# Kernel optimization log

Hardware: AMD Instinct MI355X
Metric: run time of the kernel (lower is better)

The kernel has to match this reference:

```python
import jax, jax.numpy as jnp
import numpy as np

# Module hyper-parameters (from create_with_implicit_mesh defaults)
KERNEL_RADIUS = 4
KERNEL_SIGMA2 = 0.5
EPS = 1e-8


def _forward_shift(src, flow):
    """Flow-based forward splatting with Gaussian-kernel scatter-add.

    Each source pixel at integer grid location (x, y) lands at the continuous
    target position p = (x + u, y + v). Its value is splatted onto all target
    pixels within KERNEL_RADIUS of p with weight exp(-||t - p||^2 / (2*sigma2)),
    accumulated atomically into weighted-image / weight / mask buffers.
    """
    B, C, H, W = src.shape
    HW = H * W
    R = KERNEL_RADIUS
    dt = src.dtype

    xs = jnp.arange(W, dtype=dt)
    ys = jnp.arange(H, dtype=dt)
    px = (xs[None, None, :] + flow[:, 0]).reshape(B, HW)   # continuous landing x
    py = (ys[None, :, None] + flow[:, 1]).reshape(B, HW)   # continuous landing y
    bx = jnp.floor(px).astype(jnp.int32)                   # base integer target
    by = jnp.floor(py).astype(jnp.int32)

    src_f = src.reshape(B, C, HW)
    acc_wI = jnp.zeros((B, C, HW), dt)
    acc_w = jnp.zeros((B, HW), dt)

    b2 = jnp.arange(B)[:, None]                 # (B,1) for (B,HW) scatter
    b3 = jnp.arange(B)[:, None, None]           # (B,1,1) for (B,C,HW) scatter
    c3 = jnp.arange(C)[None, :, None]           # (1,C,1)

    r2 = jnp.asarray(R * R, dt)
    for dy in range(-R, R + 1):
        for dx in range(-R, R + 1):
            tx = bx + dx
            ty = by + dy
            fx = tx.astype(dt)
            fy = ty.astype(dt)
            d2 = (fx - px) ** 2 + (fy - py) ** 2
            valid = (tx >= 0) & (tx < W) & (ty >= 0) & (ty < H) & (d2 <= r2)
            w = jnp.exp(-d2 / (2.0 * KERNEL_SIGMA2)) * valid.astype(dt)  # (B,HW)
            idx = jnp.clip(ty, 0, H - 1) * W + jnp.clip(tx, 0, W - 1)    # (B,HW)
            acc_w = acc_w.at[b2, idx].add(w)
            acc_wI = acc_wI.at[b3, c3, idx[:, None, :]].add(w[:, None, :] * src_f)

    w_img = acc_w.reshape(B, 1, H, W)
    out_img = acc_wI.reshape(B, C, H, W) / (w_img + EPS)
    mask = (w_img > 0).astype(dt)
    return out_img, mask


def setup_inputs() -> dict:
    key = jax.random.key(0)
    k1, k2 = jax.random.split(key)
    B, C, H, W = 4, 3, 720, 1280
    src_image = jax.random.normal(k1, (B, C, H, W), dtype=jnp.float32)
    flow_src_to_tar = jax.random.normal(k2, (B, 2, H, W), dtype=jnp.float32)
    return {"src_image": src_image, "flow_src_to_tar": flow_src_to_tar}


def reference(src_image, flow_src_to_tar):
    return _forward_shift(src_image, flow_src_to_tar)
```

## Files before the change

kernel.cpp:

```cpp
#include <hip/hip_runtime.h>
#include <hip/hip_fp16.h>

constexpr int B_N = 4;
constexpr int C_N = 3;
constexpr int H_IMG = 720;
constexpr int W_IMG = 1280;
constexpr int HW = H_IMG * W_IMG;

constexpr int TW = 64, TH = 64;
constexpr int HALO = 7;
constexpr int CW = TW + 2 * HALO;
constexpr int CH = TH + 2 * HALO;
constexpr int PITCH = 79;
constexpr int PLANE = CH * PITCH;
constexpr float FLOW_MAX = 3.5f;
constexpr float LOG2E = 1.44269504f;
constexpr float MARKER = 30.0f;

#define K1 0.36787944117144233f
#define K3 0.049787068367863944f
#define K5 0.006737946999085467f
#define K7 0.0009118819655545162f

__global__ __launch_bounds__(256, 2)
void gather_kernel(const float* __restrict__ src, const float* __restrict__ flow,
                   float* __restrict__ out) {
    __shared__ __half2 UV[PLANE];
    __shared__ __half2 S01[PLANE];
    __shared__ __half  S2[PLANE];

    const int b = blockIdx.z;
    const int tx0 = blockIdx.x * TW;
    const int ty0 = blockIdx.y * TH;
    const int cx0 = tx0 - HALO, cy0 = ty0 - HALO;

    const float* __restrict__ up = flow + (size_t)(b * 2) * HW;
    const float* __restrict__ vp = up + HW;
    const float* __restrict__ sp = src + (size_t)(b * 3) * HW;

    for (int idx = threadIdx.x; idx < CH * CW; idx += 256) {
        const int cr = idx / CW, cx = idx - cr * CW;
        const int gx = cx0 + cx, gy = cy0 + cr;
        float u = MARKER, v = MARKER, s0 = 0.f, s1 = 0.f, s2 = 0.f;
        if (gx >= 0 && gx < W_IMG && gy >= 0 && gy < H_IMG) {
            const int g = gy * W_IMG + gx;
            const float uu = up[g], vv = vp[g];
            if (fabsf(uu) <= FLOW_MAX && fabsf(vv) <= FLOW_MAX) {
                u = uu; v = vv;
                s0 = sp[g]; s1 = sp[HW + g]; s2 = sp[2 * HW + g];
            }
        }
        const int l = cr * PITCH + cx;
        UV[l] = __floats2half2_rn(u, v);
        S01[l] = __floats2half2_rn(s0, s1);
        S2[l] = __float2half_rn(s2);
    }
    __syncthreads();

    const int xg = threadIdx.x & 7;
    const int yg = threadIdx.x >> 3;
    const int ty_a = ty0 + 2 * yg;

    float aW[2][8], a0[2][8], a1[2][8], a2[2][8];
#pragma unroll
    for (int j = 0; j < 2; ++j)
#pragma unroll
        for (int i = 0; i < 8; ++i) { aW[j][i] = 0.f; a0[j][i] = 0.f;
                                      a1[j][i] = 0.f; a2[j][i] = 0.f; }

    for (int oy = 0; oy < 16; ++oy) {
        const float Cy = (float)(oy - 7);
        const int lrow = (2 * yg + oy) * PITCH + 8 * xg;
#pragma unroll
        for (int ox = 0; ox < 22; ++ox) {
            const int l = lrow + ox;
            const float2 uv = __half22float2(UV[l]);
            const float2 s01 = __half22float2(S01[l]);
            const float s2v = __half2float(S2[l]);

            const float dx = uv.x + (float)(ox - 11);
            const float dy = uv.y + Cy;

            const float aL = dx * LOG2E;
            const float tX = aL * dx;
            const float E  = __builtin_amdgcn_exp2f(-tX);
            const float g  = aL + aL;
            const float G  = __builtin_amdgcn_exp2f(g);
            const float Gi = __builtin_amdgcn_exp2f(-g);

            const float bL = dy * LOG2E;
            const float tY = bL * dy;
            const float eya = __builtin_amdgcn_exp2f(-tY);
            const float gy = bL + bL;
            const float Gy = __builtin_amdgcn_exp2f(gy);
            const float rk = Gy * K1;

            const float m1 = G * K1, m3 = G * K3, m5 = G * K5;
            const float n1 = Gi * K1, n3 = Gi * K3, n5 = Gi * K5, n7 = Gi * K7;
            float w[8];
            w[4] = E;
            w[5] = w[4] * m1; w[6] = w[5] * m3; w[7] = w[6] * m5;
            w[3] = w[4] * n1; w[2] = w[3] * n3; w[1] = w[2] * n5; w[0] = w[1] * n7;

            const float zw0 = eya,        zw1 = eya * rk;
            const float z00 = s01.x * eya, z01 = z00 * rk;
            const float z10 = s01.y * eya, z11 = z10 * rk;
            const float z20 = s2v * eya,   z21 = z20 * rk;

#pragma unroll
            for (int i = 0; i < 8; ++i) {
                aW[0][i] = fmaf(w[i], zw0, aW[0][i]);
                aW[1][i] = fmaf(w[i], zw1, aW[1][i]);
                a0[0][i] = fmaf(w[i], z00, a0[0][i]);
                a0[1][i] = fmaf(w[i], z01, a0[1][i]);
                a1[0][i] = fmaf(w[i], z10, a1[0][i]);
                a1[1][i] = fmaf(w[i], z11, a1[1][i]);
                a2[0][i] = fmaf(w[i], z20, a2[0][i]);
                a2[1][i] = fmaf(w[i], z21, a2[1][i]);
            }
        }
    }

    float* __restrict__ wI = out;
    float* __restrict__ wb = out + (size_t)B_N * C_N * HW;
    const int gx0 = tx0 + 8 * xg;
#pragma unroll
    for (int j = 0; j < 2; ++j) {
        const int ty = ty_a + j;
        if (ty >= H_IMG) continue;
        const int tb = ty * W_IMG + gx0;
        float* p0 = wI + (size_t)(b * 3 + 0) * HW + tb;
        float* p1 = wI + (size_t)(b * 3 + 1) * HW + tb;
        float* p2 = wI + (size_t)(b * 3 + 2) * HW + tb;
        float* pw = wb + (size_t)b * HW + tb;
        *(float4*)(p0)     = make_float4(a0[j][0], a0[j][1], a0[j][2], a0[j][3]);
        *(float4*)(p0 + 4) = make_float4(a0[j][4], a0[j][5], a0[j][6], a0[j][7]);
        *(float4*)(p1)     = make_float4(a1[j][0], a1[j][1], a1[j][2], a1[j][3]);
        *(float4*)(p1 + 4) = make_float4(a1[j][4], a1[j][5], a1[j][6], a1[j][7]);
        *(float4*)(p2)     = make_float4(a2[j][0], a2[j][1], a2[j][2], a2[j][3]);
        *(float4*)(p2 + 4) = make_float4(a2[j][4], a2[j][5], a2[j][6], a2[j][7]);
        *(float4*)(pw)     = make_float4(aW[j][0], aW[j][1], aW[j][2], aW[j][3]);
        *(float4*)(pw + 4) = make_float4(aW[j][4], aW[j][5], aW[j][6], aW[j][7]);
    }
}

__global__ __launch_bounds__(256)
void outlier_kernel(const float* __restrict__ src, const float* __restrict__ flow,
                    float* __restrict__ out) {
    const int n4 = B_N * HW / 4;
    const int i4 = blockIdx.x * 256 + threadIdx.x;
    if (i4 >= n4) return;
    const int per_b = HW / 4;
    const int b = i4 / per_b;
    const int g0 = (i4 - b * per_b) * 4;
    const float* __restrict__ up = flow + (size_t)(b * 2) * HW;
    const float4 u4 = *(const float4*)(up + g0);
    const float4 v4 = *(const float4*)(up + HW + g0);
    const float um = fmaxf(fmaxf(fabsf(u4.x), fabsf(u4.y)), fmaxf(fabsf(u4.z), fabsf(u4.w)));
    const float vm = fmaxf(fmaxf(fabsf(v4.x), fabsf(v4.y)), fmaxf(fabsf(v4.z), fabsf(v4.w)));
    if (um <= FLOW_MAX && vm <= FLOW_MAX) return;

    const float uu[4] = {u4.x, u4.y, u4.z, u4.w};
    const float vv[4] = {v4.x, v4.y, v4.z, v4.w};
    const float* __restrict__ sp = src + (size_t)(b * 3) * HW;
    float* __restrict__ wI = out;
    float* __restrict__ wb = out + (size_t)B_N * C_N * HW;

    for (int k = 0; k < 4; ++k) {
        const float u = uu[k], v = vv[k];
        if (fabsf(u) <= FLOW_MAX && fabsf(v) <= FLOW_MAX) continue;
        const int g = g0 + k;
        const int x = g % W_IMG, y = g / W_IMG;
        const float px = (float)x + u, py = (float)y + v;
        if (!(px > -6.f && px < (float)W_IMG + 5.f &&
              py > -6.f && py < (float)H_IMG + 5.f)) continue;

        const float bxf = floorf(px), byf = floorf(py);
        const int bx = (int)bxf, by = (int)byf;
        const float s0 = sp[g], s1 = sp[HW + g], s2 = sp[2 * HW + g];

        for (int dyi = -4; dyi <= 4; ++dyi) {
            const int tyy = by + dyi;
            if (tyy < 0 || tyy >= H_IMG) continue;
            const float dyf = (byf + (float)dyi) - py;
            const float dy2 = dyf * dyf;
            for (int dxi = -4; dxi <= 4; ++dxi) {
                const int txx = bx + dxi;
                if (txx < 0 || txx >= W_IMG) continue;
                const float dxf = (bxf + (float)dxi) - px;
                const float d2 = fmaf(dxf, dxf, dy2);
                if (d2 > 16.f) continue;
                const float w = __expf(-d2);
                const int t = tyy * W_IMG + txx;
                atomicAdd(&wb[(size_t)b * HW + t], w);
                atomicAdd(&wI[(size_t)(b * 3 + 0) * HW + t], w * s0);
                atomicAdd(&wI[(size_t)(b * 3 + 1) * HW + t], w * s1);
                atomicAdd(&wI[(size_t)(b * 3 + 2) * HW + t], w * s2);
            }
        }
    }
}

__global__ __launch_bounds__(256)
void finalize_kernel(float* __restrict__ out) {
    const int i = blockIdx.x * blockDim.x + threadIdx.x;
    const int n4 = B_N * HW / 4;
    if (i >= n4) return;
    const int per_b = HW / 4;
    const int b = i / per_b;
    const int hw = (i - b * per_b) * 4;
    float* __restrict__ wb = out + (size_t)B_N * C_N * HW + (size_t)b * HW + hw;
    float4 w = *(float4*)wb;
    const float4 inv = make_float4(1.f / (w.x + 1e-8f), 1.f / (w.y + 1e-8f),
                                   1.f / (w.z + 1e-8f), 1.f / (w.w + 1e-8f));
    float* base = out + (size_t)(b * 3) * HW + hw;
#pragma unroll
    for (int c = 0; c < 3; ++c) {
        float4 t = *(float4*)(base + (size_t)c * HW);
        t.x *= inv.x; t.y *= inv.y; t.z *= inv.z; t.w *= inv.w;
        *(float4*)(base + (size_t)c * HW) = t;
    }
    *(float4*)wb = make_float4(w.x > 0.f ? 1.f : 0.f, w.y > 0.f ? 1.f : 0.f,
                               w.z > 0.f ? 1.f : 0.f, w.w > 0.f ? 1.f : 0.f);
}

extern "C" void kernel_launch(void* const* d_in, const int* in_sizes, int n_in,
                              void* d_out, int out_size, void* d_ws, size_t ws_size,
                              hipStream_t stream) {
    const float* src = (const float*)d_in[0];
    const float* flow = (const float*)d_in[1];
    float* out = (float*)d_out;

    dim3 grid(W_IMG / TW, (H_IMG + TH - 1) / TH, B_N);
    gather_kernel<<<grid, 256, 0, stream>>>(src, flow, out);

    const int n4 = B_N * HW / 4;
    outlier_kernel<<<(n4 + 255) / 256, 256, 0, stream>>>(src, flow, out);
    finalize_kernel<<<(n4 + 255) / 256, 256, 0, stream>>>(out);
}
```

Measured before the change: 442.0 us.

## Use packed fp16 dot2 accumulation and a compacted outlier list

The gather inner loop now handles two source columns per step. The per-column weights and y-factors are packed into fp16 pairs with cvt_pkrtz, and the four accumulators are updated with v_dot2 (fp16 inputs, fp32 accumulate), which roughly halves the FMA count. Shared memory moves to separate fp16 planes with an even pitch so paired loads are aligned. Separately, the gather pass appends outlier pixels (flow beyond the cutoff) to a workspace list, so the outlier kernel handles only those entries instead of rescanning the whole flow field. The trade-offs are lower accuracy from fp16 products of weights and values, a global atomic counter in the load phase, an extra memset, and a fixed list capacity that silently drops outliers past the cap.

```diff
diff --git a/kernel.cpp b/kernel.cpp
--- a/kernel.cpp
+++ b/kernel.cpp
@@ -1,5 +1,4 @@
 #include <hip/hip_runtime.h>
-#include <hip/hip_fp16.h>
 
 constexpr int B_N = 4;
 constexpr int C_N = 3;
@@ -11,23 +10,24 @@
 constexpr int HALO = 7;
 constexpr int CW = TW + 2 * HALO;
 constexpr int CH = TH + 2 * HALO;
-constexpr int PITCH = 79;
+constexpr int PITCH = 80;
 constexpr int PLANE = CH * PITCH;
 constexpr float FLOW_MAX = 3.5f;
 constexpr float LOG2E = 1.44269504f;
-constexpr float MARKER = 30.0f;
+constexpr float MARKER = -30.0f;
 
 #define K1 0.36787944117144233f
 #define K3 0.049787068367863944f
 #define K5 0.006737946999085467f
 #define K7 0.0009118819655545162f
 
+typedef _Float16 h2 __attribute__((ext_vector_type(2)));
+#define PKRTZ(a, b) __builtin_bit_cast(h2, __builtin_amdgcn_cvt_pkrtz((a), (b)))
+
 __global__ __launch_bounds__(256, 2)
 void gather_kernel(const float* __restrict__ src, const float* __restrict__ flow,
-                   float* __restrict__ out) {
-    __shared__ __half2 UV[PLANE];
-    __shared__ __half2 S01[PLANE];
-    __shared__ __half  S2[PLANE];
+                   float* __restrict__ out, int* __restrict__ olist, int ocap) {
+    __shared__ _Float16 Up[PLANE], Vp[PLANE], P0[PLANE], P1[PLANE], P2[PLANE];
 
     const int b = blockIdx.z;
     const int tx0 = blockIdx.x * TW;
@@ -48,12 +48,14 @@
             if (fabsf(uu) <= FLOW_MAX && fabsf(vv) <= FLOW_MAX) {
                 u = uu; v = vv;
                 s0 = sp[g]; s1 = sp[HW + g]; s2 = sp[2 * HW + g];
+            } else if (cx >= HALO && cx < HALO + TW && cr >= HALO && cr < HALO + TH) {
+                const int k = atomicAdd(olist, 1);
+                if (k < ocap) { olist[4 + 2 * k] = b; olist[5 + 2 * k] = g; }
             }
         }
         const int l = cr * PITCH + cx;
-        UV[l] = __floats2half2_rn(u, v);
-        S01[l] = __floats2half2_rn(s0, s1);
-        S2[l] = __float2half_rn(s2);
+        Up[l] = (_Float16)u; Vp[l] = (_Float16)v;
+        P0[l] = (_Float16)s0; P1[l] = (_Float16)s1; P2[l] = (_Float16)s2;
     }
     __syncthreads();
 
@@ -72,51 +74,66 @@
         const float Cy = (float)(oy - 7);
         const int lrow = (2 * yg + oy) * PITCH + 8 * xg;
 #pragma unroll
-        for (int ox = 0; ox < 22; ++ox) {
-            const int l = lrow + ox;
-            const float2 uv = __half22float2(UV[l]);
-            const float2 s01 = __half22float2(S01[l]);
-            const float s2v = __half2float(S2[l]);
-
-            const float dx = uv.x + (float)(ox - 11);
-            const float dy = uv.y + Cy;
-
-            const float aL = dx * LOG2E;
-            const float tX = aL * dx;
-            const float E  = __builtin_amdgcn_exp2f(-tX);
-            const float g  = aL + aL;
-            const float G  = __builtin_amdgcn_exp2f(g);
-            const float Gi = __builtin_amdgcn_exp2f(-g);
-
-            const float bL = dy * LOG2E;
-            const float tY = bL * dy;
-            const float eya = __builtin_amdgcn_exp2f(-tY);
-            const float gy = bL + bL;
-            const float Gy = __builtin_amdgcn_exp2f(gy);
-            const float rk = Gy * K1;
-
-            const float m1 = G * K1, m3 = G * K3, m5 = G * K5;
-            const float n1 = Gi * K1, n3 = Gi * K3, n5 = Gi * K5, n7 = Gi * K7;
-            float w[8];
-            w[4] = E;
-            w[5] = w[4] * m1; w[6] = w[5] * m3; w[7] = w[6] * m5;
-            w[3] = w[4] * n1; w[2] = w[3] * n3; w[1] = w[2] * n5; w[0] = w[1] * n7;
-
-            const float zw0 = eya,        zw1 = eya * rk;
-            const float z00 = s01.x * eya, z01 = z00 * rk;
-            const float z10 = s01.y * eya, z11 = z10 * rk;
-            const float z20 = s2v * eya,   z21 = z20 * rk;
+        for (int oxp = 0; oxp < 11; ++oxp) {
+            const int l = lrow + 2 * oxp;
+            const h2 u2 = *(const h2*)(Up + l);
+            const h2 v2 = *(const h2*)(Vp + l);
+            const h2 s02 = *(const h2*)(P0 + l);
+            const h2 s12 = *(const h2*)(P1 + l);
+            const h2 s22 = *(const h2*)(P2 + l);
+            const float uA = (float)u2.x, uB = (float)u2.y;
+            const float vA = (float)v2.x, vB = (float)v2.y;
+
+            const float dxA = uA + (float)(2 * oxp - 11);
+            const float dxB = uB + (float)(2 * oxp - 10);
+            const float aLA = dxA * LOG2E, aLB = dxB * LOG2E;
+            const float EA = __builtin_amdgcn_exp2f(-(aLA * dxA));
+            const float EB = __builtin_amdgcn_exp2f(-(aLB * dxB));
+            const float gA = aLA + aLA, gB = aLB + aLB;
+            const float GA = __builtin_amdgcn_exp2f(gA);
+            const float GB = __builtin_amdgcn_exp2f(gB);
+            const float GiA = __builtin_amdgcn_exp2f(-gA);
+            const float GiB = __builtin_amdgcn_exp2f(-gB);
+
+            float wA[8], wB[8];
+            wA[4] = EA; wB[4] = EB;
+            wA[5] = wA[4] * (GA * K1); wB[5] = wB[4] * (GB * K1);
+            wA[6] = wA[5] * (GA * K3); wB[6] = wB[5] * (GB * K3);
+            wA[7] = wA[6] * (GA * K5); wB[7] = wB[6] * (GB * K5);
+            wA[3] = wA[4] * (GiA * K1); wB[3] = wB[4] * (GiB * K1);
+            wA[2] = wA[3] * (GiA * K3); wB[2] = wB[3] * (GiB * K3);
+            wA[1] = wA[2] * (GiA * K5); wB[1] = wB[2] * (GiB * K5);
+            wA[0] = wA[1] * (GiA * K7); wB[0] = wB[1] * (GiB * K7);
+
+            h2 w2[8];
+#pragma unroll
+            for (int i = 0; i < 8; ++i)
+                w2[i] = PKRTZ(wA[i], wB[i]);
+
+            const float dyA = vA + Cy, dyB = vB + Cy;
+            const float bLA = dyA * LOG2E, bLB = dyB * LOG2E;
+            const float eyaA = __builtin_amdgcn_exp2f(-(bLA * dyA));
+            const float eyaB = __builtin_amdgcn_exp2f(-(bLB * dyB));
+            const float rkA = __builtin_amdgcn_exp2f(bLA + bLA) * K1;
+            const float rkB = __builtin_amdgcn_exp2f(bLB + bLB) * K1;
+            const float eybA = eyaA * rkA, eybB = eyaB * rkB;
+
+            const h2 eya2 = PKRTZ(eyaA, eyaB);
+            const h2 eyb2 = PKRTZ(eybA, eybB);
+            const h2 z0a = s02 * eya2, z0b = s02 * eyb2;
+            const h2 z1a = s12 * eya2, z1b = s12 * eyb2;
+            const h2 z2a = s22 * eya2, z2b = s22 * eyb2;
 
 #pragma unroll
             for (int i = 0; i < 8; ++i) {
-                aW[0][i] = fmaf(w[i], zw0, aW[0][i]);
-                aW[1][i] = fmaf(w[i], zw1, aW[1][i]);
-                a0[0][i] = fmaf(w[i], z00, a0[0][i]);
-                a0[1][i] = fmaf(w[i], z01, a0[1][i]);
-                a1[0][i] = fmaf(w[i], z10, a1[0][i]);
-                a1[1][i] = fmaf(w[i], z11, a1[1][i]);
-                a2[0][i] = fmaf(w[i], z20, a2[0][i]);
-                a2[1][i] = fmaf(w[i], z21, a2[1][i]);
+                aW[0][i] = __builtin_amdgcn_fdot2(w2[i], eya2, aW[0][i], false);
+                aW[1][i] = __builtin_amdgcn_fdot2(w2[i], eyb2, aW[1][i], false);
+                a0[0][i] = __builtin_amdgcn_fdot2(w2[i], z0a, a0[0][i], false);
+                a0[1][i] = __builtin_amdgcn_fdot2(w2[i], z0b, a0[1][i], false);
+                a1[0][i] = __builtin_amdgcn_fdot2(w2[i], z1a, a1[0][i], false);
+                a1[1][i] = __builtin_amdgcn_fdot2(w2[i], z1b, a1[1][i], false);
+                a2[0][i] = __builtin_amdgcn_fdot2(w2[i], z2a, a2[0][i], false);
+                a2[1][i] = __builtin_amdgcn_fdot2(w2[i], z2b, a2[1][i], false);
             }
         }
     }
@@ -146,30 +163,15 @@
 
 __global__ __launch_bounds__(256)
 void outlier_kernel(const float* __restrict__ src, const float* __restrict__ flow,
-                    float* __restrict__ out) {
-    const int n4 = B_N * HW / 4;
-    const int i4 = blockIdx.x * 256 + threadIdx.x;
-    if (i4 >= n4) return;
-    const int per_b = HW / 4;
-    const int b = i4 / per_b;
-    const int g0 = (i4 - b * per_b) * 4;
-    const float* __restrict__ up = flow + (size_t)(b * 2) * HW;
-    const float4 u4 = *(const float4*)(up + g0);
-    const float4 v4 = *(const float4*)(up + HW + g0);
-    const float um = fmaxf(fmaxf(fabsf(u4.x), fabsf(u4.y)), fmaxf(fabsf(u4.z), fabsf(u4.w)));
-    const float vm = fmaxf(fmaxf(fabsf(v4.x), fabsf(v4.y)), fmaxf(fabsf(v4.z), fabsf(v4.w)));
-    if (um <= FLOW_MAX && vm <= FLOW_MAX) return;
-
-    const float uu[4] = {u4.x, u4.y, u4.z, u4.w};
-    const float vv[4] = {v4.x, v4.y, v4.z, v4.w};
-    const float* __restrict__ sp = src + (size_t)(b * 3) * HW;
+                    float* __restrict__ out, const int* __restrict__ olist, int ocap) {
+    const int count = min(olist[0], ocap);
     float* __restrict__ wI = out;
     float* __restrict__ wb = out + (size_t)B_N * C_N * HW;
-
-    for (int k = 0; k < 4; ++k) {
-        const float u = uu[k], v = vv[k];
-        if (fabsf(u) <= FLOW_MAX && fabsf(v) <= FLOW_MAX) continue;
-        const int g = g0 + k;
+    for (int e = blockIdx.x * 256 + threadIdx.x; e < count; e += gridDim.x * 256) {
+        const int b = olist[4 + 2 * e];
+        const int g = olist[5 + 2 * e];
+        const float* __restrict__ up = flow + (size_t)(b * 2) * HW;
+        const float u = up[g], v = up[HW + g];
         const int x = g % W_IMG, y = g / W_IMG;
         const float px = (float)x + u, py = (float)y + v;
         if (!(px > -6.f && px < (float)W_IMG + 5.f &&
@@ -177,6 +179,7 @@
 
         const float bxf = floorf(px), byf = floorf(py);
         const int bx = (int)bxf, by = (int)byf;
+        const float* __restrict__ sp = src + (size_t)(b * 3) * HW;
         const float s0 = sp[g], s1 = sp[HW + g], s2 = sp[2 * HW + g];
 
         for (int dyi = -4; dyi <= 4; ++dyi) {
@@ -230,11 +233,16 @@
     const float* src = (const float*)d_in[0];
     const float* flow = (const float*)d_in[1];
     float* out = (float*)d_out;
+    int* olist = (int*)d_ws;
+    const int ocap = (int)min((ws_size - 16) / 8, (size_t)1 << 20);
+
+    (void)hipMemsetAsync(d_ws, 0, 16, stream);
 
     dim3 grid(W_IMG / TW, (H_IMG + TH - 1) / TH, B_N);
-    gather_kernel<<<grid, 256, 0, stream>>>(src, flow, out);
+    gather_kernel<<<grid, 256, 0, stream>>>(src, flow, out, olist, ocap);
+
+    outlier_kernel<<<8, 256, 0, stream>>>(src, flow, out, olist, ocap);
 
     const int n4 = B_N * HW / 4;
-    outlier_kernel<<<(n4 + 255) / 256, 256, 0, stream>>>(src, flow, out);
     finalize_kernel<<<(n4 + 255) / 256, 256, 0, stream>>>(out);
 }
```

After: 530.7 us. 20.1% more time.
